# Performance work log

Hardware: AMD Instinct MI355X
Metric: run time of the kernel (lower is better)

Reference implementation:

```python
import jax, jax.numpy as jnp
import numpy as np

B, S, DM, H, FF = 2, 4096, 768, 12, 3072
WIN = 64  # one-sided window: attention_window=128 -> 64 each side
HD = DM // H


def layer_norm(x, g, b, eps=1e-5):
    mu = jnp.mean(x, axis=-1, keepdims=True)
    var = jnp.mean((x - mu) ** 2, axis=-1, keepdims=True)
    return (x - mu) / jnp.sqrt(var + eps) * g + b


def sliding_window_attention(q, k, v, w):
    # q,k,v: [B,H,S,D]; banded attention, each token sees [i-w, i+w]
    Bq, Hq, Sq, D = q.shape
    nc = Sq // w
    qc = (q * (1.0 / np.sqrt(D))).reshape(Bq, Hq, nc, w, D)
    kp = jnp.pad(k, ((0, 0), (0, 0), (w, w), (0, 0)))
    vp = jnp.pad(v, ((0, 0), (0, 0), (w, w), (0, 0)))
    # overlapping key windows of length 3w per query chunk
    idx = jnp.arange(nc)[:, None] * w + jnp.arange(3 * w)[None, :]  # [nc,3w]
    kw = kp[:, :, idx]  # [B,H,nc,3w,D]
    vw = vp[:, :, idx]
    scores = jnp.einsum('bhcqd,bhckd->bhcqk', qc, kw)  # [B,H,nc,w,3w]
    i = jnp.arange(w)[:, None]
    j = jnp.arange(3 * w)[None, :]
    band = (j >= i) & (j <= i + 2 * w)  # |rel pos| <= w
    gpos = jnp.arange(nc)[:, None, None] * w - w + j[None, :, :]  # key global pos [nc,1,3w]
    valid = band[None, :, :] & (gpos >= 0) & (gpos < Sq)  # [nc,w,3w]
    scores = jnp.where(valid[None, None], scores, -jnp.inf)
    probs = jax.nn.softmax(scores, axis=-1)
    out = jnp.einsum('bhcqk,bhckd->bhcqd', probs, vw)
    return out.reshape(Bq, Hq, Sq, D)


def setup_inputs() -> dict:
    key = jax.random.key(0)
    ks = jax.random.split(key, 8)
    sd = 1.0 / np.sqrt(DM)
    return {
        'x': jax.random.normal(ks[0], (B, S, DM), jnp.float32),
        'Wq': jax.random.normal(ks[1], (DM, DM), jnp.float32) * sd,
        'bq': jnp.zeros((DM,), jnp.float32),
        'Wk': jax.random.normal(ks[2], (DM, DM), jnp.float32) * sd,
        'bk': jnp.zeros((DM,), jnp.float32),
        'Wv': jax.random.normal(ks[3], (DM, DM), jnp.float32) * sd,
        'bv': jnp.zeros((DM,), jnp.float32),
        'ln1_g': jnp.ones((DM,), jnp.float32),
        'ln1_b': jnp.zeros((DM,), jnp.float32),
        'W1': jax.random.normal(ks[4], (DM, FF), jnp.float32) * sd,
        'b1': jnp.zeros((FF,), jnp.float32),
        'W2': jax.random.normal(ks[5], (FF, DM), jnp.float32) * (1.0 / np.sqrt(FF)),
        'b2': jnp.zeros((DM,), jnp.float32),
        'ln2_g': jnp.ones((DM,), jnp.float32),
        'ln2_b': jnp.zeros((DM,), jnp.float32),
    }


def reference(x, Wq, bq, Wk, bk, Wv, bv, ln1_g, ln1_b, W1, b1, W2, b2, ln2_g, ln2_b):
    Bx, Sx, d = x.shape

    def split_heads(t):
        return t.reshape(Bx, Sx, H, HD).transpose(0, 2, 1, 3)

    q = split_heads(x @ Wq + bq)
    k = split_heads(x @ Wk + bk)
    v = split_heads(x @ Wv + bv)
    attn = sliding_window_attention(q, k, v, WIN)  # [B,H,S,D]
    attn = attn.transpose(0, 2, 1, 3).reshape(Bx, Sx, d)
    # Longformer self-attention here has no output projection; residual directly
    x1 = layer_norm(attn + x, ln1_g, ln1_b)
    ff = jax.nn.gelu(x1 @ W1 + b1) @ W2 + b2
    return layer_norm(ff + x1, ln2_g, ln2_b)
```

## Files before the change

### kernel.cpp

```cpp
#include <hip/hip_runtime.h>
#include <cstdint>
#include <cstddef>

#define S_LEN   4096
#define D_MODEL 768
#define N_HEADS 12
#define HEAD_DIM 64
#define FF_DIM  3072
#define B_SZ    2
#define M_ROWS  (B_SZ * S_LEN)
#define QKV_N   (3 * D_MODEL)

typedef unsigned short u16;
typedef __attribute__((ext_vector_type(8))) __bf16 bf16x8;
typedef __attribute__((ext_vector_type(4))) float  f32x4;

__device__ __forceinline__ float bf2f(u16 u) {
    union { unsigned u32; float f; } cv; cv.u32 = ((unsigned)u) << 16; return cv.f;
}
__device__ __forceinline__ u16 f2bf(float f) {
    __bf16 b = (__bf16)f;
    union { __bf16 b; u16 u; } cv; cv.b = b; return cv.u;
}
__device__ __forceinline__ float gelu_fast(float x) {
    float x2 = x * x;
    float u  = x * fmaf(0.035677408f, x2, 0.7978845608f);
    float e  = __expf(-2.f * u);
    return x * __builtin_amdgcn_rcpf(1.f + e);
}
__device__ __forceinline__ void async16(const void* g, void* l) {
    __builtin_amdgcn_global_load_lds(
        (const __attribute__((address_space(1))) unsigned int*)g,
        (__attribute__((address_space(3))) unsigned int*)l, 16, 0, 0);
}

__global__ __launch_bounds__(256) void prep(
    const float* __restrict__ x,
    const float* __restrict__ Wq, const float* __restrict__ Wk,
    const float* __restrict__ Wv,
    const float* __restrict__ W1, const float* __restrict__ W2,
    const float* __restrict__ bq, const float* __restrict__ bk,
    const float* __restrict__ bv,
    u16* __restrict__ xbf, u16* __restrict__ WqkvT, u16* __restrict__ W1T,
    u16* __restrict__ W2T, float* __restrict__ biasqkv)
{
    __shared__ __align__(16) u16 T[64 * 72];
    const int id = blockIdx.x;
    const int t = threadIdx.x;

    if (id < 1584) {
        const float* in; u16* o_; int C, R, tx, ty;
        if (id < 432) {
            const int z = id / 144, tile = id % 144;
            in = (z == 0) ? Wq : (z == 1) ? Wk : Wv;
            o_ = WqkvT + (size_t)z * 768 * 768;
            R = 768; C = 768; tx = tile % 12; ty = tile / 12;
        } else if (id < 1008) {
            const int tile = id - 432;
            in = W1; o_ = W1T; R = 768; C = 3072; tx = tile % 48; ty = tile / 48;
        } else {
            const int tile = id - 1008;
            in = W2; o_ = W2T; R = 3072; C = 768; tx = tile % 12; ty = tile / 12;
        }
        const int r0 = ty * 64, c0 = tx * 64;
        for (int v = t; v < 512; v += 256) {
            int rr = v >> 3, c8 = (v & 7) * 8;
            const float* p = in + (size_t)(r0 + rr) * C + c0 + c8;
            float4 a = *(const float4*)p;
            float4 b = *(const float4*)(p + 4);
            union { uint4 q; u16 el[8]; } o;
            o.el[0] = f2bf(a.x); o.el[1] = f2bf(a.y);
            o.el[2] = f2bf(a.z); o.el[3] = f2bf(a.w);
            o.el[4] = f2bf(b.x); o.el[5] = f2bf(b.y);
            o.el[6] = f2bf(b.z); o.el[7] = f2bf(b.w);
            *(uint4*)&T[rr * 72 + c8] = o.q;
        }
        __syncthreads();
        for (int v = t; v < 512; v += 256) {
            int cc = v >> 3, r8 = (v & 7) * 8;
            union { uint4 q; u16 el[8]; } tmp;
            #pragma unroll
            for (int e = 0; e < 8; ++e) tmp.el[e] = T[(r8 + e) * 72 + cc];
            *(uint4*)&o_[(size_t)(c0 + cc) * R + r0 + r8] = tmp.q;
        }
    } else if (id == 1584) {
        for (int i = t; i < 768; i += 256) {
            biasqkv[i]        = bq[i];
            biasqkv[768 + i]  = bk[i];
            biasqkv[1536 + i] = bv[i];
        }
    } else {
        const long c = id - 1585;
        #pragma unroll
        for (int j = 0; j < 4; ++j) {
            const long i = c * 1024 + j * 256 + t;
            const float* p = x + i * 8;
            float4 a = *(const float4*)p;
            float4 b = *(const float4*)(p + 4);
            union { uint4 q; u16 el[8]; } o;
            o.el[0] = f2bf(a.x); o.el[1] = f2bf(a.y);
            o.el[2] = f2bf(a.z); o.el[3] = f2bf(a.w);
            o.el[4] = f2bf(b.x); o.el[5] = f2bf(b.y);
            o.el[6] = f2bf(b.z); o.el[7] = f2bf(b.w);
            ((uint4*)xbf)[i] = o.q;
        }
    }
}

template<int MI>
__global__ __launch_bounds__(256) void gemm_bt_t(const u16* __restrict__ A,
                                                 const u16* __restrict__ BT,
                                                 const float* __restrict__ bias,
                                                 void* __restrict__ C,
                                                 int M, int N, int K, int act, int ofp32)
{
    constexpr int TM = MI * 32;
    __shared__ __align__(16) u16 SM[TM * 64 + 128 * 64];
    u16* As = SM;
    u16* Bs = SM + TM * 64;
    const int t = threadIdx.x;

    const int NX = gridDim.x, MY8 = gridDim.y >> 3;
    const int L = blockIdx.y * NX + blockIdx.x;
    const int xcd = L & 7, q = L >> 3;
    const long m0 = (long)(xcd * MY8 + q / NX) * TM;
    const long n0 = (long)(q % NX) * 128;

    const int lane = t & 63, w = t >> 6;
    const int wm = (w >> 1) * (MI * 16), wn = (w & 1) * 64;
    const int lr = lane & 15, lq = lane >> 4;

    const int r0 = t >> 3;
    const int cg = ((t & 7) ^ (r0 & 7)) * 8;
    const u16* pa = &A[(m0 + r0) * (long)K + cg];
    const u16* pb = &BT[(n0 + r0) * (long)K + cg];
    char* la = (char*)As + t * 16;
    char* lb = (char*)Bs + t * 16;

    f32x4 acc[MI][4] = {};

    for (int k0 = 0; k0 < K; k0 += 64) {
        #pragma unroll
        for (int p = 0; p < MI; ++p)
            async16(pa + k0 + p * 32 * (long)K, la + p * 4096);
        #pragma unroll
        for (int p = 0; p < 4; ++p)
            async16(pb + k0 + p * 32 * (long)K, lb + p * 4096);
        __syncthreads();
        #pragma unroll
        for (int ks = 0; ks < 2; ++ks) {
            const int kc = ((ks * 4 + lq) ^ (lr & 7)) * 8;
            bf16x8 af[MI], bfr[4];
            #pragma unroll
            for (int mi = 0; mi < MI; ++mi)
                af[mi] = *(const bf16x8*)&As[(wm + mi * 16 + lr) * 64 + kc];
            #pragma unroll
            for (int ni = 0; ni < 4; ++ni)
                bfr[ni] = *(const bf16x8*)&Bs[(wn + ni * 16 + lr) * 64 + kc];
            #pragma unroll
            for (int mi = 0; mi < MI; ++mi)
                #pragma unroll
                for (int ni = 0; ni < 4; ++ni)
                    acc[mi][ni] = __builtin_amdgcn_mfma_f32_16x16x32_bf16(
                        af[mi], bfr[ni], acc[mi][ni], 0, 0, 0);
        }
        __syncthreads();
    }

    if (ofp32) {
        #pragma unroll
        for (int mi = 0; mi < MI; ++mi) {
            #pragma unroll
            for (int ni = 0; ni < 4; ++ni) {
                const long colg = n0 + wn + ni * 16 + lr;
                const float bv = bias[colg];
                #pragma unroll
                for (int r = 0; r < 4; ++r) {
                    const long row = m0 + wm + mi * 16 + lq * 4 + r;
                    float v = acc[mi][ni][r] + bv;
                    if (act == 1) v = gelu_fast(v);
                    ((float*)C)[row * (long)N + colg] = v;
                }
            }
        }
    } else {
        u16* Cs = SM;
        #pragma unroll
        for (int mi = 0; mi < MI; ++mi) {
            #pragma unroll
            for (int ni = 0; ni < 4; ++ni) {
                const int col = wn + ni * 16 + lr;
                const float bv = bias[n0 + col];
                #pragma unroll
                for (int r = 0; r < 4; ++r) {
                    const int row = wm + mi * 16 + lq * 4 + r;
                    float v = acc[mi][ni][r] + bv;
                    if (act == 1) v = gelu_fast(v);
                    Cs[row * 128 + col] = f2bf(v);
                }
            }
        }
        __syncthreads();
        #pragma unroll
        for (int i = 0; i < MI * 2; ++i) {
            const int v = i * 256 + t;
            const int row = v >> 4, c8 = (v & 15) * 8;
            uint4 qv = *(const uint4*)&Cs[row * 128 + c8];
            *(uint4*)&((u16*)C)[(m0 + row) * (long)N + n0 + c8] = qv;
        }
    }
}

__global__ __launch_bounds__(256) void attn_mfma(const u16* __restrict__ qkv,
                                                 u16* __restrict__ attn_out)
{
    const int c = blockIdx.x;
    const int h = blockIdx.y;
    const int b = blockIdx.z;
    const int t = threadIdx.x;
    const int wave = t >> 6, lane = t & 63;
    const int lr = lane & 15, lq = lane >> 4;

    __shared__ __align__(16) u16 Ps[64 * 200];
    __shared__ __align__(16) u16 VT[64 * 200];
    __shared__ float linv[64];

    const long base = (long)b * S_LEN;
    const long qrow0 = base + c * 64;

    for (int v = t; v < 1536; v += 256) {
        int j = v >> 3, d8 = (v & 7) * 8;
        int s = c * 64 - 64 + j;
        int scl = s < 0 ? 0 : (s > S_LEN - 1 ? S_LEN - 1 : s);
        uint4 raw = *(const uint4*)&qkv[(base + scl) * (long)QKV_N + 2 * D_MODEL + h * 64 + d8];
        union { uint4 q; u16 el[8]; } u; u.q = raw;
        #pragma unroll
        for (int e = 0; e < 8; ++e) VT[(d8 + e) * 200 + j] = u.el[e];
    }

    bf16x8 aq[2];
    #pragma unroll
    for (int ks = 0; ks < 2; ++ks)
        aq[ks] = *(const bf16x8*)&qkv[(qrow0 + wave * 16 + lr) * (long)QKV_N
                                      + h * 64 + ks * 32 + lq * 8];

    f32x4 sacc[12];
    #pragma unroll
    for (int nt = 0; nt < 12; ++nt) {
        int key = nt * 16 + lr;
        int s = c * 64 - 64 + key;
        int scl = s < 0 ? 0 : (s > S_LEN - 1 ? S_LEN - 1 : s);
        const u16* kp = &qkv[(base + scl) * (long)QKV_N + D_MODEL + h * 64 + lq * 8];
        bf16x8 bk0 = *(const bf16x8*)kp;
        bf16x8 bk1 = *(const bf16x8*)(kp + 32);
        f32x4 z = {0.f, 0.f, 0.f, 0.f};
        z = __builtin_amdgcn_mfma_f32_16x16x32_bf16(aq[0], bk0, z, 0, 0, 0);
        z = __builtin_amdgcn_mfma_f32_16x16x32_bf16(aq[1], bk1, z, 0, 0, 0);
        sacc[nt] = z;
    }

    float m[4] = {-1e30f, -1e30f, -1e30f, -1e30f};
    #pragma unroll
    for (int nt = 0; nt < 12; ++nt) {
        const int j = nt * 16 + lr;
        const int gpos = c * 64 - 64 + j;
        #pragma unroll
        for (int r = 0; r < 4; ++r) {
            const int qi = wave * 16 + lq * 4 + r;
            const bool ok = (j >= qi) && (j <= qi + 128) && (gpos >= 0) && (gpos < S_LEN);
            const float v = ok ? sacc[nt][r] * 0.125f : -1e30f;
            sacc[nt][r] = v;
            m[r] = fmaxf(m[r], v);
        }
    }
    #pragma unroll
    for (int o = 1; o < 16; o <<= 1)
        #pragma unroll
        for (int r = 0; r < 4; ++r) m[r] = fmaxf(m[r], __shfl_xor(m[r], o));

    float sum[4] = {0.f, 0.f, 0.f, 0.f};
    #pragma unroll
    for (int nt = 0; nt < 12; ++nt)
        #pragma unroll
        for (int r = 0; r < 4; ++r) {
            const float e = __expf(sacc[nt][r] - m[r]);
            sacc[nt][r] = e;
            sum[r] += e;
        }
    #pragma unroll
    for (int o = 1; o < 16; o <<= 1)
        #pragma unroll
        for (int r = 0; r < 4; ++r) sum[r] += __shfl_xor(sum[r], o);

    #pragma unroll
    for (int nt = 0; nt < 12; ++nt)
        #pragma unroll
        for (int r = 0; r < 4; ++r)
            Ps[(wave * 16 + lq * 4 + r) * 200 + nt * 16 + lr] = f2bf(sacc[nt][r]);
    if (lr == 0) {
        #pragma unroll
        for (int r = 0; r < 4; ++r)
            linv[wave * 16 + lq * 4 + r] = 1.f / sum[r];
    }
    __syncthreads();

    f32x4 oacc[4] = {};
    #pragma unroll
    for (int ks = 0; ks < 6; ++ks) {
        bf16x8 ap = *(const bf16x8*)&Ps[(wave * 16 + lr) * 200 + ks * 32 + lq * 8];
        #pragma unroll
        for (int nt = 0; nt < 4; ++nt) {
            bf16x8 bv = *(const bf16x8*)&VT[(nt * 16 + lr) * 200 + ks * 32 + lq * 8];
            oacc[nt] = __builtin_amdgcn_mfma_f32_16x16x32_bf16(ap, bv, oacc[nt], 0, 0, 0);
        }
    }

    __syncthreads();
    u16* Os = VT;
    #pragma unroll
    for (int nt = 0; nt < 4; ++nt) {
        #pragma unroll
        for (int r = 0; r < 4; ++r) {
            const int row = wave * 16 + lq * 4 + r;
            Os[row * 72 + nt * 16 + lr] = f2bf(oacc[nt][r] * linv[row]);
        }
    }
    __syncthreads();
    #pragma unroll
    for (int i = 0; i < 2; ++i) {
        const int v = i * 256 + t;
        const int row = v >> 3, c8 = (v & 7) * 8;
        uint4 qv = *(const uint4*)&Os[row * 72 + c8];
        *(uint4*)&attn_out[(qrow0 + row) * (long)D_MODEL + h * 64 + c8] = qv;
    }
}

__global__ __launch_bounds__(256) void ln_kernel(const void* a, int af32,
                                                 const u16* __restrict__ b,
                                                 const float* __restrict__ g,
                                                 const float* __restrict__ beta,
                                                 void* out, int of32)
{
    const int t = threadIdx.x;
    const int wv = t >> 6, lane = t & 63;
    const long r = (long)blockIdx.x * 4 + wv;
    const long rb = r * D_MODEL;

    float v[12];
    float s = 0.f, s2 = 0.f;
    #pragma unroll
    for (int k = 0; k < 3; ++k) {
        const long e0 = rb + k * 256 + lane * 4;
        float xa[4];
        if (af32) {
            float4 fa = *(const float4*)((const float*)a + e0);
            xa[0] = fa.x; xa[1] = fa.y; xa[2] = fa.z; xa[3] = fa.w;
        } else {
            union { uint2 u; u16 el[4]; } ua;
            ua.u = *(const uint2*)((const u16*)a + e0);
            #pragma unroll
            for (int j = 0; j < 4; ++j) xa[j] = bf2f(ua.el[j]);
        }
        union { uint2 u; u16 el[4]; } ub;
        ub.u = *(const uint2*)(b + e0);
        #pragma unroll
        for (int j = 0; j < 4; ++j) {
            const float xx = xa[j] + bf2f(ub.el[j]);
            v[k * 4 + j] = xx; s += xx; s2 += xx * xx;
        }
    }
    #pragma unroll
    for (int o = 32; o > 0; o >>= 1) {
        s  += __shfl_xor(s, o);
        s2 += __shfl_xor(s2, o);
    }
    const float mu   = s * (1.f / 768.f);
    const float var  = s2 * (1.f / 768.f) - mu * mu;
    const float rstd = rsqrtf(var + 1e-5f);

    #pragma unroll
    for (int k = 0; k < 3; ++k) {
        const long col = k * 256 + lane * 4;
        float4 g4 = *(const float4*)(g + col);
        float4 b4 = *(const float4*)(beta + col);
        float o0 = (v[k*4+0] - mu) * rstd * g4.x + b4.x;
        float o1 = (v[k*4+1] - mu) * rstd * g4.y + b4.y;
        float o2 = (v[k*4+2] - mu) * rstd * g4.z + b4.z;
        float o3 = (v[k*4+3] - mu) * rstd * g4.w + b4.w;
        if (of32) {
            float4 ov = {o0, o1, o2, o3};
            *(float4*)((float*)out + rb + col) = ov;
        } else {
            union { uint2 u; u16 el[4]; } uo;
            uo.el[0] = f2bf(o0); uo.el[1] = f2bf(o1);
            uo.el[2] = f2bf(o2); uo.el[3] = f2bf(o3);
            *(uint2*)((u16*)out + rb + col) = uo.u;
        }
    }
}

extern "C" void kernel_launch(void* const* d_in, const int* in_sizes, int n_in,
                              void* d_out, int out_size, void* d_ws, size_t ws_size,
                              hipStream_t stream)
{
    const float* x    = (const float*)d_in[0];
    const float* Wq   = (const float*)d_in[1];
    const float* bq   = (const float*)d_in[2];
    const float* Wk   = (const float*)d_in[3];
    const float* bk   = (const float*)d_in[4];
    const float* Wv   = (const float*)d_in[5];
    const float* bv   = (const float*)d_in[6];
    const float* ln1g = (const float*)d_in[7];
    const float* ln1b = (const float*)d_in[8];
    const float* W1   = (const float*)d_in[9];
    const float* b1   = (const float*)d_in[10];
    const float* W2   = (const float*)d_in[11];
    const float* b2   = (const float*)d_in[12];
    const float* ln2g = (const float*)d_in[13];
    const float* ln2b = (const float*)d_in[14];

    char* ws = (char*)d_ws;
    size_t off = 0;
    u16* WqkvT  = (u16*)(ws + off);   off += (size_t)QKV_N * D_MODEL * 2;
    u16* W1T    = (u16*)(ws + off);   off += (size_t)FF_DIM * D_MODEL * 2;
    u16* W2T    = (u16*)(ws + off);   off += (size_t)D_MODEL * FF_DIM * 2;
    float* biasqkv = (float*)(ws + off); off += (size_t)QKV_N * 4;
    u16* big    = (u16*)(ws + off);   off += (size_t)M_ROWS * FF_DIM * 2;
    u16* x1     = (u16*)(ws + off);   off += (size_t)M_ROWS * D_MODEL * 2;

    u16* xbf    = big;
    u16* qkv    = big + (size_t)M_ROWS * D_MODEL;
    u16* hbuf   = big;
    u16* attnb  = (u16*)d_out;
    float* outf = (float*)d_out;

    dim3 blk(256);
    prep<<<dim3(2353), blk, 0, stream>>>(x, Wq, Wk, Wv, W1, W2, bq, bk, bv,
                                         xbf, WqkvT, W1T, W2T, biasqkv);

    gemm_bt_t<4><<<dim3(QKV_N / 128, M_ROWS / 128), blk, 0, stream>>>(
        xbf, WqkvT, biasqkv, qkv, M_ROWS, QKV_N, D_MODEL, 0, 0);
    attn_mfma<<<dim3(64, N_HEADS, B_SZ), blk, 0, stream>>>(qkv, attnb);
    ln_kernel<<<dim3(M_ROWS / 4), blk, 0, stream>>>(attnb, 0, xbf, ln1g, ln1b, x1, 0);
    gemm_bt_t<4><<<dim3(FF_DIM / 128, M_ROWS / 128), blk, 0, stream>>>(
        x1, W1T, b1, hbuf, M_ROWS, FF_DIM, D_MODEL, 1, 0);
    gemm_bt_t<2><<<dim3(D_MODEL / 128, M_ROWS / 64), blk, 0, stream>>>(
        hbuf, W2T, b2, outf, M_ROWS, D_MODEL, FF_DIM, 0, 1);
    ln_kernel<<<dim3(M_ROWS / 4), blk, 0, stream>>>(outf, 1, x1, ln2g, ln2b, outf, 1);
}
```

Before: 308.7 us.

## Double-buffer GEMM LDS tiles and XOR-swizzle transpose/VT shared memory

The GEMM main loop now keeps two LDS buffers and issues the async loads for the next K tile while the MFMAs run on the current one, so global-load latency overlaps with compute. The weight-transpose staging tile and the attention V-transpose buffer use an XOR swizzle on 8-element column groups to reduce LDS bank conflicts on their strided scalar writes and reads. Double buffering doubles the GEMM's LDS footprint, which may reduce occupancy, and the loop tail (not shown) has to keep the sync placement correct.

After: 318.8 us. +3.3%, slower.

```diff
diff --git a/kernel.cpp b/kernel.cpp
--- a/kernel.cpp
+++ b/kernel.cpp
@@ -64,8 +64,8 @@
         }
         const int r0 = ty * 64, c0 = tx * 64;
         for (int v = t; v < 512; v += 256) {
-            int rr = v >> 3, c8 = (v & 7) * 8;
-            const float* p = in + (size_t)(r0 + rr) * C + c0 + c8;
+            int rr = v >> 3, c8c = v & 7;
+            const float* p = in + (size_t)(r0 + rr) * C + c0 + c8c * 8;
             float4 a = *(const float4*)p;
             float4 b = *(const float4*)(p + 4);
             union { uint4 q; u16 el[8]; } o;
@@ -73,14 +73,15 @@
             o.el[2] = f2bf(a.z); o.el[3] = f2bf(a.w);
             o.el[4] = f2bf(b.x); o.el[5] = f2bf(b.y);
             o.el[6] = f2bf(b.z); o.el[7] = f2bf(b.w);
-            *(uint4*)&T[rr * 72 + c8] = o.q;
+            *(uint4*)&T[rr * 72 + ((c8c ^ (rr >> 3)) * 8)] = o.q;
         }
         __syncthreads();
         for (int v = t; v < 512; v += 256) {
-            int cc = v >> 3, r8 = (v & 7) * 8;
+            int cc = v >> 3, r8 = (v & 7) * 8, a = v & 7;
+            const int cbase = (((cc >> 3) ^ a) * 8) + (cc & 7);
             union { uint4 q; u16 el[8]; } tmp;
             #pragma unroll
-            for (int e = 0; e < 8; ++e) tmp.el[e] = T[(r8 + e) * 72 + cc];
+            for (int e = 0; e < 8; ++e) tmp.el[e] = T[(r8 + e) * 72 + cbase];
             *(uint4*)&o_[(size_t)(c0 + cc) * R + r0 + r8] = tmp.q;
         }
     } else if (id == 1584) {
@@ -115,9 +116,8 @@
                                                  int M, int N, int K, int act, int ofp32)
 {
     constexpr int TM = MI * 32;
-    __shared__ __align__(16) u16 SM[TM * 64 + 128 * 64];
-    u16* As = SM;
-    u16* Bs = SM + TM * 64;
+    constexpr int HALF = TM * 64 + 128 * 64;
+    __shared__ __align__(16) u16 SM[2 * HALF];
     const int t = threadIdx.x;
 
     const int NX = gridDim.x, MY8 = gridDim.y >> 3;
@@ -134,19 +134,34 @@
     const int cg = ((t & 7) ^ (r0 & 7)) * 8;
     const u16* pa = &A[(m0 + r0) * (long)K + cg];
     const u16* pb = &BT[(n0 + r0) * (long)K + cg];
-    char* la = (char*)As + t * 16;
-    char* lb = (char*)Bs + t * 16;
 
     f32x4 acc[MI][4] = {};
-
-    for (int k0 = 0; k0 < K; k0 += 64) {
-        #pragma unroll
-        for (int p = 0; p < MI; ++p)
-            async16(pa + k0 + p * 32 * (long)K, la + p * 4096);
-        #pragma unroll
-        for (int p = 0; p < 4; ++p)
-            async16(pb + k0 + p * 32 * (long)K, lb + p * 4096);
-        __syncthreads();
+    const int NT = K >> 6;
+
+    {
+        char* la = (char*)SM + t * 16;
+        char* lb = (char*)(SM + TM * 64) + t * 16;
+        #pragma unroll
+        for (int p = 0; p < MI; ++p) async16(pa + p * 32 * (long)K, la + p * 4096);
+        #pragma unroll
+        for (int p = 0; p < 4; ++p)  async16(pb + p * 32 * (long)K, lb + p * 4096);
+    }
+    __syncthreads();
+
+    for (int kt = 0; kt < NT; ++kt) {
+        const u16* As = SM + (kt & 1) * HALF;
+        const u16* Bs = As + TM * 64;
+
+        if (kt + 1 < NT) {
+            char* la = (char*)(SM + ((kt + 1) & 1) * HALF) + t * 16;
+            char* lb = la + TM * 64 * 2;
+            const long kn = (long)(kt + 1) * 64;
+            #pragma unroll
+            for (int p = 0; p < MI; ++p) async16(pa + kn + p * 32 * (long)K, la + p * 4096);
+            #pragma unroll
+            for (int p = 0; p < 4; ++p)  async16(pb + kn + p * 32 * (long)K, lb + p * 4096);
+        }
+
         #pragma unroll
         for (int ks = 0; ks < 2; ++ks) {
             const int kc = ((ks * 4 + lq) ^ (lr & 7)) * 8;
@@ -234,8 +249,10 @@
         int scl = s < 0 ? 0 : (s > S_LEN - 1 ? S_LEN - 1 : s);
         uint4 raw = *(const uint4*)&qkv[(base + scl) * (long)QKV_N + 2 * D_MODEL + h * 64 + d8];
         union { uint4 q; u16 el[8]; } u; u.q = raw;
-        #pragma unroll
-        for (int e = 0; e < 8; ++e) VT[(d8 + e) * 200 + j] = u.el[e];
+        const int pc = ((j >> 3) & ~7) | (((j >> 3) & 7) ^ (v & 7));
+        const int cbase = pc * 8 + (j & 7);
+        #pragma unroll
+        for (int e = 0; e < 8; ++e) VT[(d8 + e) * 200 + cbase] = u.el[e];
     }
 
     bf16x8 aq[2];
@@ -310,7 +327,10 @@
         bf16x8 ap = *(const bf16x8*)&Ps[(wave * 16 + lr) * 200 + ks * 32 + lq * 8];
         #pragma unroll
         for (int nt = 0; nt < 4; ++nt) {
-            bf16x8 bv = *(const bf16x8*)&VT[(nt * 16 + lr) * 200 + ks * 32 + lq * 8];
+            const int rowd = nt * 16 + lr;
+            const int lc = 4 * ks + lq;
+            const int pc = (lc & ~7) | ((lc & 7) ^ (rowd >> 3));
+            bf16x8 bv = *(const bf16x8*)&VT[rowd * 200 + pc * 8];
             oacc[nt] = __builtin_amdgcn_mfma_f32_16x16x32_bf16(ap, bv, oacc[nt], 0, 0, 0);
         }
     }
```
